# Performance work log

Measured on AMD Instinct MI355X. Metric: run time of the kernel, lower is better.

Reference implementation:

```python
import jax, jax.numpy as jnp
import numpy as np

MUL = 16            # multiplicity of 0e and 1o irreps (in and out)
N_NODES = 10000
N_EDGES = 160000
EDGE_FDIM = 128
H_DIM = 128
WNUM = 4 * MUL * MUL  # 4 instructions x (16 u x 1 v x 16 w) = 1024 weights per edge


def setup_inputs() -> dict:
    key = jax.random.key(0)
    ks = jax.random.split(key, 6)
    x = jax.random.normal(ks[0], (N_NODES, 4 * MUL), dtype=jnp.float32)  # 16x0e + 16x1o -> dim 64
    edge_index = jax.random.randint(ks[1], (2, N_EDGES), 0, N_NODES, dtype=jnp.int32)
    edge_attr = jax.random.normal(ks[2], (N_EDGES, EDGE_FDIM), dtype=jnp.float32)
    edge_sh = jax.random.normal(ks[3], (N_EDGES, 4), dtype=jnp.float32)  # 1x0e + 1x1o
    fc_w1 = jax.random.normal(ks[4], (EDGE_FDIM, H_DIM), dtype=jnp.float32) / np.sqrt(EDGE_FDIM)
    fc_b1 = jnp.zeros((H_DIM,), jnp.float32)
    fc_w2 = jax.random.normal(ks[5], (H_DIM, WNUM), dtype=jnp.float32) / np.sqrt(H_DIM)
    fc_b2 = jnp.zeros((WNUM,), jnp.float32)
    return dict(x=x, edge_index=edge_index, edge_attr=edge_attr, edge_sh=edge_sh,
                fc_w1=fc_w1, fc_b1=fc_b1, fc_w2=fc_w2, fc_b2=fc_b2)


def _tensor_product(xe, edge_sh, w):
    """FullyConnectedTensorProduct('16x0e+16x1o', '1x0e+1x1o', '16x0e+16x1o'),
    shared_weights=False. Instructions (uvw, v=1):
      0e x 0e -> 0e ; 0e x 1o -> 1o ; 1o x 0e -> 1o ; 1o x 1o -> 0e (dot / sqrt(3)).
    Path alpha = 1/sqrt(fan_in) with fan_in = 2*MUL per output irrep (2 paths x 16x1)."""
    x0 = xe[:, :MUL]                          # [E, 16] scalars
    x1 = xe[:, MUL:].reshape(-1, MUL, 3)      # [E, 16, 3] vectors
    sh0 = edge_sh[:, 0:1]                     # [E, 1]
    sh1 = edge_sh[:, 1:4]                     # [E, 3]
    wp = w.reshape(-1, 4, MUL, MUL)           # [E, 4 paths, u, w]
    w00, w01, w10, w11 = wp[:, 0], wp[:, 1], wp[:, 2], wp[:, 3]
    alpha = 1.0 / np.sqrt(2.0 * MUL)
    dot = jnp.einsum('eum,em->eu', x1, sh1)   # 1o . 1o -> 0e
    out0 = alpha * (jnp.einsum('eu,euw->ew', x0 * sh0, w00)
                    + jnp.einsum('eu,euw->ew', dot, w11) / np.sqrt(3.0))  # [E, 16]
    out1 = alpha * (jnp.einsum('eu,euw,em->ewm', x0, w01, sh1)
                    + jnp.einsum('eum,euw->ewm', x1 * sh0[:, :, None], w10))  # [E, 16, 3]
    return jnp.concatenate([out0, out1.reshape(-1, 3 * MUL)], axis=-1)  # [E, 64]


def reference(x, edge_index, edge_attr, edge_sh, fc_w1, fc_b1, fc_w2, fc_b2):
    src, dst = edge_index[0], edge_index[1]
    # per-edge tensor-product weights from edge features (dropout p=0 -> identity)
    w = jax.nn.relu(edge_attr @ fc_w1 + fc_b1) @ fc_w2 + fc_b2       # [E, 1024]
    tp_out = _tensor_product(x[src], edge_sh, w)                      # gather + TP
    seg = jax.ops.segment_sum(tp_out, dst, num_segments=N_NODES)      # scatter-add
    cnt = jax.ops.segment_sum(jnp.ones((N_EDGES,), tp_out.dtype), dst, num_segments=N_NODES)
    out = seg / jnp.maximum(cnt, 1.0)[:, None]                        # mean aggregation
    # residual: out_dim == in_dim (64), so F.pad is a no-op
    return out + x
```

## Files before the change

kernel.cpp:

```cpp
#include <hip/hip_runtime.h>
#include <stdint.h>

#define E_TOTAL 160000
#define NODES   10000
#define FDIM    128
#define HDIM    128
#define WN      1024
#define CDIM    64
#define EPB     32
#define NTHR    256

typedef __bf16 bf16x8 __attribute__((ext_vector_type(8)));
typedef __bf16 bf16x4 __attribute__((ext_vector_type(4)));
typedef float  f32x4  __attribute__((ext_vector_type(4)));

#define MFMA16(a,b,c) __builtin_amdgcn_mfma_f32_16x16x32_bf16(a,b,c,0,0,0)

#define WS_W1B (512*1024)
#define WS_CNT (576*1024)

__device__ __forceinline__ f32x4 ntload4(const float* p) {
    return __builtin_nontemporal_load((const f32x4*)p);
}

__global__ void prep_kernel(const float* __restrict__ W1, const float* __restrict__ W2,
                            __bf16* __restrict__ W1B, __bf16* __restrict__ W2B,
                            float* __restrict__ out_acc, int* __restrict__ cnt) {
    const int b   = blockIdx.x;
    const int tid = threadIdx.x;
    if (b < 72) {
        const float* W = (b < 64) ? W2 : W1;
        __bf16* outB   = (b < 64) ? W2B : W1B;
        const int N    = (b < 64) ? WN : HDIM;
        const int tile = (b < 64) ? b : (b - 64);
        const int lane = tid & 63, ks = tid >> 6;
        const int n  = tile * 16 + (lane & 15);
        const int k0 = ks * 32 + (lane >> 4) * 8;
        bf16x8 hi;
        #pragma unroll
        for (int j = 0; j < 8; ++j) hi[j] = (__bf16)W[(size_t)(k0 + j) * N + n];
        *(bf16x8*)(outB + ((size_t)(tile * 4 + ks) * 64 + lane) * 8) = hi;
    } else {
        const int zt = (b - 72) * NTHR + tid;
        const float4 z4 = make_float4(0.f, 0.f, 0.f, 0.f);
        for (int i = zt; i < NODES * CDIM / 4; i += 8 * NTHR) ((float4*)out_acc)[i] = z4;
        for (int i = zt; i < NODES; i += 8 * NTHR) cnt[i] = 0;
    }
}

__global__ __launch_bounds__(NTHR, 4)
void fused_edge_kernel(const float* __restrict__ x,
                       const int*   __restrict__ edge_index,
                       const float* __restrict__ edge_attr,
                       const float* __restrict__ edge_sh,
                       const float* __restrict__ fc_b1,
                       const float* __restrict__ fc_b2,
                       const __bf16* __restrict__ W1B,
                       const __bf16* __restrict__ W2B,
                       float* __restrict__ out_acc,
                       int*   __restrict__ cnt)
{
    __shared__ float s_f[6][16][EPB];
    __shared__ __align__(16) char s_ab[16384];
    __shared__ float s_b2s[WN];
    __shared__ float s_sh1[3][36];
    __shared__ int   s_dst[EPB];

    __bf16* s_attr = (__bf16*)s_ab;
    __bf16* s_h    = (__bf16*)(s_ab + 8192);

    const int tid  = threadIdx.x;
    const int w    = tid >> 6;
    const int th   = w >> 1;
    const int kh   = w & 1;
    const int lane = tid & 63;
    const int quad = lane >> 4;
    const int li   = lane & 15;
    const int e0   = blockIdx.x * EPB;

    if (lane < 32) {
        const int e  = lane;
        const int up = w * 4;
        const int ge = e0 + e;
        const int src = edge_index[ge];
        const f32x4 sh4 = ntload4(edge_sh + (size_t)ge * 4);
        if (tid < EPB) {
            const int d = edge_index[E_TOTAL + ge];
            s_dst[e] = d;
            atomicAdd(&cnt[d], 1);
            s_sh1[0][e] = sh4.y; s_sh1[1][e] = sh4.z; s_sh1[2][e] = sh4.w;
        }
        const float* xp = x + (size_t)src * CDIM;
        const float4 x0v = *(const float4*)(xp + up);
        const float4 xa  = *(const float4*)(xp + 16 + up * 3);
        const float4 xb  = *(const float4*)(xp + 16 + up * 3 + 4);
        const float4 xc  = *(const float4*)(xp + 16 + up * 3 + 8);
        const float x1v[4][3] = {
            {xa.x, xa.y, xa.z}, {xa.w, xb.x, xb.y},
            {xb.z, xb.w, xc.x}, {xc.y, xc.z, xc.w}};
        const float x0a[4] = {x0v.x, x0v.y, x0v.z, x0v.w};
        const float alpha = 0.17677669529663689f;
        const float ai3   = alpha * 0.57735026918962576f;
        const float sh0 = sh4.x;
        #pragma unroll
        for (int j = 0; j < 4; ++j) {
            const int u = up + j;
            const float x0u = x0a[j];
            s_f[0][u][e] = alpha * sh0 * x0u;
            s_f[1][u][e] = alpha * x0u;
            s_f[2][u][e] = alpha * sh0 * x1v[j][0];
            s_f[3][u][e] = alpha * sh0 * x1v[j][1];
            s_f[4][u][e] = alpha * sh0 * x1v[j][2];
            s_f[5][u][e] = ai3 * (x1v[j][0]*sh4.y + x1v[j][1]*sh4.z + x1v[j][2]*sh4.w);
        }
    }
    #pragma unroll
    for (int t4 = 0; t4 < 4; ++t4) {
        const int t = tid + t4 * NTHR;
        const int e = t >> 5, i4 = t & 31;
        const f32x4 v = ntload4(edge_attr + (size_t)(e0 + e) * FDIM + i4 * 4);
        const int f = i4 >> 3, j0 = (i4 & 1) * 4, qc = (i4 >> 1) & 3;
        const int g = e >> 4, lc = e & 15;
        bf16x4 bv = {(__bf16)v[0], (__bf16)v[1], (__bf16)v[2], (__bf16)v[3]};
        *(bf16x4*)(s_attr + (((f * 2 + g) * 64 + qc * 16 + lc) * 8 + j0)) = bv;
    }
    *(f32x4*)&s_b2s[tid * 4] = *(const f32x4*)(fc_b2 + tid * 4);
    __syncthreads();

    {
        const int nt0 = w * 2;
        const float b1a = fc_b1[nt0 * 16 + li];
        const float b1b = fc_b1[(nt0 + 1) * 16 + li];
        bf16x8 A1[2][4];
        #pragma unroll
        for (int g = 0; g < 2; ++g)
            #pragma unroll
            for (int ks = 0; ks < 4; ++ks)
                A1[g][ks] = *(const bf16x8*)(s_attr + ((ks * 2 + g) * 64 + lane) * 8);
        #pragma unroll
        for (int nt2 = 0; nt2 < 2; ++nt2) {
            const int nt = nt0 + nt2;
            const float bias = nt2 ? b1b : b1a;
            bf16x8 Bf[4];
            #pragma unroll
            for (int ks = 0; ks < 4; ++ks)
                Bf[ks] = *(const bf16x8*)(W1B + ((size_t)(nt * 4 + ks) * 64 + lane) * 8);
            f32x4 acc[2];
            #pragma unroll
            for (int g = 0; g < 2; ++g) acc[g] = (f32x4){bias, bias, bias, bias};
            #pragma unroll
            for (int ks = 0; ks < 4; ++ks)
                #pragma unroll
                for (int g = 0; g < 2; ++g) acc[g] = MFMA16(A1[g][ks], Bf[ks], acc[g]);
            const int f  = nt >> 1;
            const int qc = (2 * (nt & 1) + (li >> 3)) & 3;
            const int j  = li & 7;
            #pragma unroll
            for (int g = 0; g < 2; ++g)
                #pragma unroll
                for (int r = 0; r < 4; ++r)
                    s_h[((f * 2 + g) * 64 + qc * 16 + (quad * 4 + r)) * 8 + j] =
                        (__bf16)fmaxf(acc[g][r], 0.f);
        }
    }
    __syncthreads();

    bf16x8 A2[2][2];
    #pragma unroll
    for (int g = 0; g < 2; ++g)
        #pragma unroll
        for (int k2 = 0; k2 < 2; ++k2)
            A2[g][k2] = *(const bf16x8*)(s_h + (((kh * 2 + k2) * 2 + g) * 64 + lane) * 8);

    f32x4 o0[2];
    f32x4 o1[2][3];
    #pragma unroll
    for (int g = 0; g < 2; ++g) {
        o0[g] = (f32x4){0.f, 0.f, 0.f, 0.f};
        #pragma unroll
        for (int m = 0; m < 3; ++m) o1[g][m] = (f32x4){0.f, 0.f, 0.f, 0.f};
    }
    const int tbase = th * 32;
    const __bf16* Wp = W2B + ((size_t)(tbase * 4 + kh * 2) * 64 + lane) * 8;
    bf16x8 P[2][2];
    #pragma unroll
    for (int s = 0; s < 2; ++s)
        #pragma unroll
        for (int k2 = 0; k2 < 2; ++k2)
            P[s][k2] = *(const bf16x8*)(Wp + (s * 4 + k2) * 512);

    #pragma unroll
    for (int half = 0; half < 2; ++half) {
        #pragma unroll
        for (int cc = 0; cc < 16; ++cc) {
            const int c = half * 16 + cc;
            const int u = cc;
            const bf16x8 b0 = P[c & 1][0];
            const bf16x8 b1 = P[c & 1][1];
            if (c + 2 < 32) {
                #pragma unroll
                for (int k2 = 0; k2 < 2; ++k2)
                    P[c & 1][k2] = *(const bf16x8*)(Wp + ((c + 2) * 4 + k2) * 512);
            }
            f32x4 acc[2];
            if (kh == 0) {
                const float b2v = s_b2s[(tbase + c) * 16 + li];
                acc[0] = (f32x4){b2v, b2v, b2v, b2v};
                acc[1] = acc[0];
            } else {
                acc[0] = (f32x4){0.f, 0.f, 0.f, 0.f};
                acc[1] = acc[0];
            }
            #pragma unroll
            for (int g = 0; g < 2; ++g) {
                acc[g] = MFMA16(A2[g][0], b0, acc[g]);
                acc[g] = MFMA16(A2[g][1], b1, acc[g]);
            }
            if (th == 0) {
                if (half == 0) {
                    #pragma unroll
                    for (int g = 0; g < 2; ++g)
                        o0[g] += *(const f32x4*)&s_f[0][u][g * 16 + quad * 4] * acc[g];
                } else {
                    #pragma unroll
                    for (int g = 0; g < 2; ++g)
                        o1[g][0] += *(const f32x4*)&s_f[1][u][g * 16 + quad * 4] * acc[g];
                }
            } else {
                if (half == 0) {
                    #pragma unroll
                    for (int g = 0; g < 2; ++g)
                        #pragma unroll
                        for (int m = 0; m < 3; ++m)
                            o1[g][m] += *(const f32x4*)&s_f[2 + m][u][g * 16 + quad * 4] * acc[g];
                } else {
                    #pragma unroll
                    for (int g = 0; g < 2; ++g)
                        o0[g] += *(const f32x4*)&s_f[5][u][g * 16 + quad * 4] * acc[g];
                }
            }
        }
    }
    if (th == 0) {
        #pragma unroll
        for (int g = 0; g < 2; ++g) {
            const f32x4 t1 = o1[g][0];
            o1[g][2] = t1 * *(const f32x4*)&s_sh1[2][g * 16 + quad * 4];
            o1[g][1] = t1 * *(const f32x4*)&s_sh1[1][g * 16 + quad * 4];
            o1[g][0] = t1 * *(const f32x4*)&s_sh1[0][g * 16 + quad * 4];
        }
    }

    __syncthreads();
    float* regA = (float*)s_ab;
    float* regB = (float*)(s_ab + 8192);
    float* regC = &s_f[0][0][0];
    float* dump = (kh == 1) ? ((th == 0) ? regA : regB) : ((th == 1) ? regC : nullptr);
    if (dump) {
        #pragma unroll
        for (int g = 0; g < 2; ++g)
            #pragma unroll
            for (int r = 0; r < 4; ++r) {
                float* row = dump + (g * 16 + quad * 4 + r) * 64;
                row[li] = o0[g][r];
                #pragma unroll
                for (int m = 0; m < 3; ++m) row[16 + li * 3 + m] = o1[g][m][r];
            }
    }
    __syncthreads();
    if (kh == 0 && th == 0) {
        #pragma unroll
        for (int g = 0; g < 2; ++g)
            #pragma unroll
            for (int r = 0; r < 4; ++r) {
                const int e = g * 16 + quad * 4 + r;
                const float* rA = regA + e * 64;
                const float* rB = regB + e * 64;
                const float* rC = regC + e * 64;
                float* op = out_acc + (size_t)s_dst[e] * CDIM;
                unsafeAtomicAdd(&op[li], o0[g][r] + rA[li] + rB[li] + rC[li]);
                #pragma unroll
                for (int m = 0; m < 3; ++m) {
                    const int s = 16 + li * 3 + m;
                    unsafeAtomicAdd(&op[s], o1[g][m][r] + rA[s] + rB[s] + rC[s]);
                }
            }
    }
}

__global__ void finalize_kernel(const float* __restrict__ x,
                                const int*   __restrict__ cnt,
                                float*       __restrict__ out)
{
    const int idx = blockIdx.x * blockDim.x + threadIdx.x;
    if (idx < NODES * CDIM) {
        const int n = idx >> 6;
        const float c = (float)(cnt[n] > 1 ? cnt[n] : 1);
        out[idx] = out[idx] / c + x[idx];
    }
}

extern "C" void kernel_launch(void* const* d_in, const int* in_sizes, int n_in,
                              void* d_out, int out_size, void* d_ws, size_t ws_size,
                              hipStream_t stream) {
    (void)in_sizes; (void)n_in; (void)out_size; (void)ws_size;
    const float* x          = (const float*)d_in[0];
    const int*   edge_index = (const int*)  d_in[1];
    const float* edge_attr  = (const float*)d_in[2];
    const float* edge_sh    = (const float*)d_in[3];
    const float* fc_w1      = (const float*)d_in[4];
    const float* fc_b1      = (const float*)d_in[5];
    const float* fc_w2      = (const float*)d_in[6];
    const float* fc_b2      = (const float*)d_in[7];
    float*  out = (float*)d_out;
    __bf16* W2B = (__bf16*)d_ws;
    __bf16* W1B = (__bf16*)((char*)d_ws + WS_W1B);
    int*    cnt = (int*)((char*)d_ws + WS_CNT);

    prep_kernel<<<80, NTHR, 0, stream>>>(fc_w1, fc_w2, W1B, W2B, out, cnt);
    fused_edge_kernel<<<E_TOTAL / EPB, NTHR, 0, stream>>>(
        x, edge_index, edge_attr, edge_sh, fc_b1, fc_b2, W1B, W2B, out, cnt);
    finalize_kernel<<<(NODES * CDIM + NTHR - 1) / NTHR, NTHR, 0, stream>>>(x, cnt, out);
}
```

Baseline: 252.0 us.

## Split final reduction and atomics across two waves, pad LDS, deepen W2 prefetch

Shared memory is merged into one pooled buffer so the cross-wave reduction buffers can use padded row strides (66, 17, 49) that avoid LDS bank conflicts. The final atomic scatter is split between two waves: one handles the scalar outputs and the other the vector outputs, where before a single wave issued all 64 atomics per edge. The W2 register prefetch ring grows from 2 to 4 slots to hide more global-load latency. The larger ring raises register pressure, which may hurt occupancy under launch_bounds(256,4).

```diff
diff --git a/kernel.cpp b/kernel.cpp
--- a/kernel.cpp
+++ b/kernel.cpp
@@ -60,14 +60,14 @@
                        float* __restrict__ out_acc,
                        int*   __restrict__ cnt)
 {
-    __shared__ float s_f[6][16][EPB];
-    __shared__ __align__(16) char s_ab[16384];
-    __shared__ float s_b2s[WN];
+    __shared__ __align__(16) char s_pool[32768];
     __shared__ float s_sh1[3][36];
     __shared__ int   s_dst[EPB];
 
-    __bf16* s_attr = (__bf16*)s_ab;
-    __bf16* s_h    = (__bf16*)(s_ab + 8192);
+    float*  s_f    = (float*)s_pool;
+    __bf16* s_attr = (__bf16*)(s_pool + 12288);
+    __bf16* s_h    = (__bf16*)(s_pool + 20480);
+    float*  s_b2s  = (float*)(s_pool + 28672);
 
     const int tid  = threadIdx.x;
     const int w    = tid >> 6;
@@ -106,12 +106,12 @@
         for (int j = 0; j < 4; ++j) {
             const int u = up + j;
             const float x0u = x0a[j];
-            s_f[0][u][e] = alpha * sh0 * x0u;
-            s_f[1][u][e] = alpha * x0u;
-            s_f[2][u][e] = alpha * sh0 * x1v[j][0];
-            s_f[3][u][e] = alpha * sh0 * x1v[j][1];
-            s_f[4][u][e] = alpha * sh0 * x1v[j][2];
-            s_f[5][u][e] = ai3 * (x1v[j][0]*sh4.y + x1v[j][1]*sh4.z + x1v[j][2]*sh4.w);
+            s_f[(0 * 16 + u) * 32 + e] = alpha * sh0 * x0u;
+            s_f[(1 * 16 + u) * 32 + e] = alpha * x0u;
+            s_f[(2 * 16 + u) * 32 + e] = alpha * sh0 * x1v[j][0];
+            s_f[(3 * 16 + u) * 32 + e] = alpha * sh0 * x1v[j][1];
+            s_f[(4 * 16 + u) * 32 + e] = alpha * sh0 * x1v[j][2];
+            s_f[(5 * 16 + u) * 32 + e] = ai3 * (x1v[j][0]*sh4.y + x1v[j][1]*sh4.z + x1v[j][2]*sh4.w);
         }
     }
     #pragma unroll
@@ -182,9 +182,9 @@
     }
     const int tbase = th * 32;
     const __bf16* Wp = W2B + ((size_t)(tbase * 4 + kh * 2) * 64 + lane) * 8;
-    bf16x8 P[2][2];
-    #pragma unroll
-    for (int s = 0; s < 2; ++s)
+    bf16x8 P[4][2];
+    #pragma unroll
+    for (int s = 0; s < 4; ++s)
         #pragma unroll
         for (int k2 = 0; k2 < 2; ++k2)
             P[s][k2] = *(const bf16x8*)(Wp + (s * 4 + k2) * 512);
@@ -195,12 +195,12 @@
         for (int cc = 0; cc < 16; ++cc) {
             const int c = half * 16 + cc;
             const int u = cc;
-            const bf16x8 b0 = P[c & 1][0];
-            const bf16x8 b1 = P[c & 1][1];
-            if (c + 2 < 32) {
+            const bf16x8 b0 = P[c & 3][0];
+            const bf16x8 b1 = P[c & 3][1];
+            if (c + 4 < 32) {
                 #pragma unroll
                 for (int k2 = 0; k2 < 2; ++k2)
-                    P[c & 1][k2] = *(const bf16x8*)(Wp + ((c + 2) * 4 + k2) * 512);
+                    P[c & 3][k2] = *(const bf16x8*)(Wp + ((c + 4) * 4 + k2) * 512);
             }
             f32x4 acc[2];
             if (kh == 0) {
@@ -220,11 +220,11 @@
                 if (half == 0) {
                     #pragma unroll
                     for (int g = 0; g < 2; ++g)
-                        o0[g] += *(const f32x4*)&s_f[0][u][g * 16 + quad * 4] * acc[g];
+                        o0[g] += *(const f32x4*)&s_f[(0 * 16 + u) * 32 + g * 16 + quad * 4] * acc[g];
                 } else {
                     #pragma unroll
                     for (int g = 0; g < 2; ++g)
-                        o1[g][0] += *(const f32x4*)&s_f[1][u][g * 16 + quad * 4] * acc[g];
+                        o1[g][0] += *(const f32x4*)&s_f[(1 * 16 + u) * 32 + g * 16 + quad * 4] * acc[g];
                 }
             } else {
                 if (half == 0) {
@@ -232,11 +232,11 @@
                     for (int g = 0; g < 2; ++g)
                         #pragma unroll
                         for (int m = 0; m < 3; ++m)
-                            o1[g][m] += *(const f32x4*)&s_f[2 + m][u][g * 16 + quad * 4] * acc[g];
+                            o1[g][m] += *(const f32x4*)&s_f[((2 + m) * 16 + u) * 32 + g * 16 + quad * 4] * acc[g];
                 } else {
                     #pragma unroll
                     for (int g = 0; g < 2; ++g)
-                        o0[g] += *(const f32x4*)&s_f[5][u][g * 16 + quad * 4] * acc[g];
+                        o0[g] += *(const f32x4*)&s_f[(5 * 16 + u) * 32 + g * 16 + quad * 4] * acc[g];
                 }
             }
         }
@@ -252,19 +252,34 @@
     }
 
     __syncthreads();
-    float* regA = (float*)s_ab;
-    float* regB = (float*)(s_ab + 8192);
-    float* regC = &s_f[0][0][0];
-    float* dump = (kh == 1) ? ((th == 0) ? regA : regB) : ((th == 1) ? regC : nullptr);
-    if (dump) {
+    float* dA = (float*)s_pool;
+    float* dB = (float*)(s_pool + 8448);
+    float* dC = (float*)(s_pool + 16896);
+    float* dD = (float*)(s_pool + 19072);
+    if (kh == 1) {
+        float* base = (th == 0) ? dA : dB;
         #pragma unroll
         for (int g = 0; g < 2; ++g)
             #pragma unroll
             for (int r = 0; r < 4; ++r) {
-                float* row = dump + (g * 16 + quad * 4 + r) * 64;
+                float* row = base + (g * 16 + quad * 4 + r) * 66;
                 row[li] = o0[g][r];
                 #pragma unroll
                 for (int m = 0; m < 3; ++m) row[16 + li * 3 + m] = o1[g][m][r];
+            }
+    } else if (th == 1) {
+        #pragma unroll
+        for (int g = 0; g < 2; ++g)
+            #pragma unroll
+            for (int r = 0; r < 4; ++r)
+                dC[(g * 16 + quad * 4 + r) * 17 + li] = o0[g][r];
+    } else {
+        #pragma unroll
+        for (int g = 0; g < 2; ++g)
+            #pragma unroll
+            for (int r = 0; r < 4; ++r) {
+                float* row = dD + (g * 16 + quad * 4 + r) * 49 + li * 3;
+                row[0] = o1[g][0][r]; row[1] = o1[g][1][r]; row[2] = o1[g][2][r];
             }
     }
     __syncthreads();
@@ -274,16 +289,22 @@
             #pragma unroll
             for (int r = 0; r < 4; ++r) {
                 const int e = g * 16 + quad * 4 + r;
-                const float* rA = regA + e * 64;
-                const float* rB = regB + e * 64;
-                const float* rC = regC + e * 64;
-                float* op = out_acc + (size_t)s_dst[e] * CDIM;
-                unsafeAtomicAdd(&op[li], o0[g][r] + rA[li] + rB[li] + rC[li]);
-                #pragma unroll
-                for (int m = 0; m < 3; ++m) {
-                    const int s = 16 + li * 3 + m;
-                    unsafeAtomicAdd(&op[s], o1[g][m][r] + rA[s] + rB[s] + rC[s]);
-                }
+                const float v = o0[g][r] + dA[e * 66 + li] + dB[e * 66 + li] + dC[e * 17 + li];
+                unsafeAtomicAdd(out_acc + (size_t)s_dst[e] * CDIM + li, v);
+            }
+    } else if (kh == 0 && th == 1) {
+        #pragma unroll
+        for (int g = 0; g < 2; ++g)
+            #pragma unroll
+            for (int r = 0; r < 4; ++r) {
+                const int e = g * 16 + quad * 4 + r;
+                float* op = out_acc + (size_t)s_dst[e] * CDIM + 16 + li * 3;
+                const float* rA = dA + e * 66 + 16 + li * 3;
+                const float* rB = dB + e * 66 + 16 + li * 3;
+                const float* rD = dD + e * 49 + li * 3;
+                #pragma unroll
+                for (int m = 0; m < 3; ++m)
+                    unsafeAtomicAdd(op + m, o1[g][m][r] + rA[m] + rB[m] + rD[m]);
             }
     }
 }
```

Measured after the change: 253.3 us. No clear change (+0.5%).
